# Kernel optimization log

Measured on AMD Instinct MI355X. Metric: run time of the kernel, lower is better.

The kernel has to match this reference:

```python
import jax, jax.numpy as jnp
import numpy as np

H = 8          # attention heads
L = 2          # gnn_layers
D = 256        # embedding_size (= per-head out channels)
NEG_SLOPE = 0.2
LN_EPS = 1e-5


def setup_inputs() -> dict:
    key = jax.random.key(0)
    ks = jax.random.split(key, 10)
    B, N, E = 8, 4096, 131072
    node_embeddings = jax.random.normal(ks[0], (B, N, D), dtype=jnp.float32)
    edges = jax.random.randint(ks[1], (B, 2, E), 0, N, dtype=jnp.int64)
    s = 1.0 / np.sqrt(D)
    W       = jax.random.normal(ks[2], (L, H * D, D), dtype=jnp.float32) * s   # GATConv lin weight
    att_src = jax.random.normal(ks[3], (L, H, D), dtype=jnp.float32) * s
    att_dst = jax.random.normal(ks[4], (L, H, D), dtype=jnp.float32) * s
    gat_bias = jnp.zeros((L, H * D), dtype=jnp.float32)
    lin_W   = jax.random.normal(ks[5], (L, D, H * D), dtype=jnp.float32) * (1.0 / np.sqrt(H * D))
    lin_b   = jnp.zeros((L, D), dtype=jnp.float32)
    ln_gamma = jnp.ones((D,), dtype=jnp.float32)
    ln_beta  = jnp.zeros((D,), dtype=jnp.float32)
    return {"node_embeddings": node_embeddings, "edges": edges, "W": W,
            "att_src": att_src, "att_dst": att_dst, "gat_bias": gat_bias,
            "lin_W": lin_W, "lin_b": lin_b, "ln_gamma": ln_gamma, "ln_beta": ln_beta}


def _gat_conv(x, edge_index, Wl, a_src, a_dst, bias):
    # x: [N, D]; edge_index: [2, E] (row0 = src j, row1 = dst i)
    N = x.shape[0]
    loops = jnp.arange(N, dtype=edge_index.dtype)
    src = jnp.concatenate([edge_index[0], loops])   # PyG add_self_loops=True
    dst = jnp.concatenate([edge_index[1], loops])
    h = (x @ Wl.T).reshape(N, H, D)                 # [N, H, D]
    a_s = jnp.sum(h * a_src, axis=-1)               # [N, H]
    a_d = jnp.sum(h * a_dst, axis=-1)               # [N, H]
    e = jax.nn.leaky_relu(a_s[src] + a_d[dst], NEG_SLOPE)   # [E+N, H]
    # softmax over incoming edges of each destination node
    emax = jax.ops.segment_max(e, dst, num_segments=N)
    ex = jnp.exp(e - emax[dst])
    denom = jax.ops.segment_sum(ex, dst, num_segments=N)
    alpha = ex / (denom[dst] + 1e-16)               # [E+N, H]
    msg = h[src] * alpha[:, :, None]                # [E+N, H, D]
    out = jax.ops.segment_sum(msg, dst, num_segments=N)     # [N, H, D]
    return out.reshape(N, H * D) + bias


def _layer_norm(x, gamma, beta):
    mu = jnp.mean(x, axis=-1, keepdims=True)
    var = jnp.mean(jnp.square(x - mu), axis=-1, keepdims=True)
    return (x - mu) * jax.lax.rsqrt(var + LN_EPS) * gamma + beta


def reference(node_embeddings, edges, W, att_src, att_dst, gat_bias, lin_W, lin_b, ln_gamma, ln_beta):
    def per_graph(x, ei):
        h = x
        for l in range(L):
            res = h
            g = _gat_conv(h, ei, W[l], att_src[l], att_dst[l], gat_bias[l])
            g = g @ lin_W[l].T + lin_b[l]
            g = _layer_norm(g, ln_gamma, ln_beta)
            h = jax.nn.relu(g + res)   # dropout is identity at inference
        return h
    return jax.vmap(per_graph)(node_embeddings, edges)
```

## Files before the change

### kernel.cpp

```cpp
#include <hip/hip_runtime.h>
#include <hip/hip_bf16.h>

#define BB 8
#define NN 4096
#define EE 131072
#define ENL (EE + NN)
#define DD 256
#define HH 8
#define HD 2048
#define NPB (BB * NN)
#define CHUNK 16384
#define CAP 128

typedef __attribute__((ext_vector_type(8))) short bf16x8;
typedef __attribute__((ext_vector_type(4))) float f32x4;

static __device__ __forceinline__ float bf_lo(unsigned int u) { return __uint_as_float(u << 16); }
static __device__ __forceinline__ float bf_hi(unsigned int u) { return __uint_as_float(u & 0xFFFF0000u); }
static __device__ __forceinline__ unsigned short f2bf(float f) {
    __hip_bfloat16 h = __float2bfloat16(f);
    return *reinterpret_cast<unsigned short*>(&h);
}
static __device__ __forceinline__ unsigned int pack2(float a, float b) {
    return ((unsigned)f2bf(b) << 16) | f2bf(a);
}
static __device__ __forceinline__ void load_lds16(const void* g, void* l) {
    __builtin_amdgcn_global_load_lds(
        (const __attribute__((address_space(1))) unsigned int*)(g),
        (__attribute__((address_space(3))) unsigned int*)(l), 16, 0, 0);
}
static __device__ __forceinline__ float rl_f(float v, int lane) {
    return __uint_as_float(__builtin_amdgcn_readlane(__float_as_uint(v), lane));
}

__global__ void k_scatter(const int* __restrict__ edges, int* __restrict__ cnt, int* __restrict__ col) {
    int b = blockIdx.y;
    int idx = blockIdx.x * 256 + threadIdx.x;
    if (idx >= ENL) return;
    int src, dst;
    if (idx < EE) { src = edges[b*2*EE + idx]; dst = edges[b*2*EE + EE + idx]; }
    else { src = dst = idx - EE; }
    int g = b * NN + dst;
    int pos = atomicAdd(&cnt[g], 1);
    if (pos < CAP) col[(size_t)g * CAP + pos] = src;
}

__global__ __launch_bounds__(256) void k_prepA(const float* __restrict__ W, const float* __restrict__ linW,
                                               unsigned short* __restrict__ M2t,
                                               const float* __restrict__ asrc, const float* __restrict__ adst,
                                               float* __restrict__ wsatt, float* __restrict__ wdatt) {
    __shared__ float red[2][4][64];
    int bx = blockIdx.x;
    if (bx < 512) {
        int cb = bx & 31, h = (bx >> 5) & 7, l = bx >> 8;
        int d = threadIdx.x;
        const float* Bp = W + ((size_t)l * HD + h * DD) * DD;
        const float* Ap = linW + ((size_t)l * DD + cb * 8) * HD + h * DD;
        float acc[8] = {};
        for (int o = 0; o < DD; ++o) {
            float w = Bp[(size_t)o * DD + d];
            #pragma unroll
            for (int c = 0; c < 8; ++c)
                acc[c] = fmaf(Ap[(size_t)c * HD + o], w, acc[c]);
        }
        #pragma unroll
        for (int c = 0; c < 8; ++c)
            M2t[((size_t)l * DD + cb * 8 + c) * HD + h * DD + d] = f2bf(acc[c]);
    } else {
        int idx = bx - 512;
        int kb = idx & 3, h = (idx >> 2) & 7, l = idx >> 5;
        int k = threadIdx.x & 63, dg = threadIdx.x >> 6;
        float accs = 0.f, accd = 0.f;
        #pragma unroll 4
        for (int dd = 0; dd < 64; ++dd) {
            int d = dg * 64 + dd;
            float w = W[((size_t)l * HD + h * DD + d) * DD + kb * 64 + k];
            accs = fmaf(asrc[(l*HH + h)*DD + d], w, accs);
            accd = fmaf(adst[(l*HH + h)*DD + d], w, accd);
        }
        red[0][dg][k] = accs; red[1][dg][k] = accd;
        __syncthreads();
        int t = threadIdx.x;
        if (t < 64)
            wsatt[(l*HH + h)*DD + kb*64 + t] = red[0][0][t] + red[0][1][t] + red[0][2][t] + red[0][3][t];
        else if (t < 128) {
            int kk = t - 64;
            wdatt[(l*HH + h)*DD + kb*64 + kk] = red[1][0][kk] + red[1][1][kk] + red[1][2][kk] + red[1][3][kk];
        }
    }
}

__global__ __launch_bounds__(256) void k_prepB(const float* __restrict__ gbias, const float* __restrict__ linW,
                                               const float* __restrict__ linb, float* __restrict__ bias2,
                                               const float* __restrict__ ws, const float* __restrict__ wd,
                                               unsigned short* __restrict__ frag) {
    int bx = blockIdx.x;
    if (bx < 128) {
        int wv = threadIdx.x >> 6, lane = threadIdx.x & 63;
        int o = bx * 4 + wv;
        int l = o >> 8, c = o & 255;
        const float4* g4 = (const float4*)(gbias + l * HD);
        const float4* w4 = (const float4*)(linW + (size_t)l * DD * HD + (size_t)c * HD);
        float acc = 0.f;
        #pragma unroll
        for (int j = 0; j < 8; ++j) {
            float4 g = g4[j * 64 + lane]; float4 w = w4[j * 64 + lane];
            acc += g.x * w.x + g.y * w.y + g.z * w.z + g.w * w.w;
        }
        #pragma unroll
        for (int msk = 1; msk < 64; msk <<= 1) acc += __shfl_xor(acc, msk);
        if (lane == 0) bias2[o] = acc + linb[o];
    } else {
        int idx = bx - 128;
        int l = idx >> 1;
        int t = (idx & 1) * 256 + threadIdx.x;
        int ks = t >> 6, lane = t & 63, c = lane & 15, q = lane >> 4;
        #pragma unroll
        for (int j = 0; j < 8; ++j) {
            int k = ks * 32 + q * 8 + j;
            float v = (c < 8) ? ws[(l*HH + c)*DD + k] : wd[(l*HH + (c-8))*DD + k];
            frag[((size_t)l * 512 + t) * 8 + j] = f2bf(v);
        }
    }
}

__global__ void k_tobf(const float* __restrict__ X, uint2* __restrict__ xb2) {
    int idx = blockIdx.x * 256 + threadIdx.x;
    float4 v = *(const float4*)(X + (size_t)idx * 4);
    uint2 o; o.x = pack2(v.x, v.y); o.y = pack2(v.z, v.w);
    xb2[idx] = o;
}

__global__ __launch_bounds__(256) void k_attn_mfma(const unsigned short* __restrict__ xb,
                                                   const unsigned short* __restrict__ attfrag,
                                                   float* __restrict__ a_s, float* __restrict__ a_d) {
    int tid = threadIdx.x;
    int wv = tid >> 6, lane = tid & 63;
    int m0 = blockIdx.x * 64 + wv * 16;
    int c = lane & 15, q = lane >> 4;
    const unsigned short* arow = xb + (size_t)(m0 + c) * DD;
    f32x4 acc = (f32x4){0.f, 0.f, 0.f, 0.f};
    #pragma unroll
    for (int ks = 0; ks < 8; ++ks) {
        bf16x8 af = *(const bf16x8*)(arow + ks * 32 + q * 8);
        bf16x8 bf = *(const bf16x8*)(attfrag + (size_t)(ks * 64 + lane) * 8);
        acc = __builtin_amdgcn_mfma_f32_16x16x32_bf16(af, bf, acc, 0, 0, 0);
    }
    #pragma unroll
    for (int rg = 0; rg < 4; ++rg) {
        int row = m0 + q * 4 + rg;
        if (c < 8) a_s[row * 8 + c] = acc[rg];
        else       a_d[row * 8 + (c - 8)] = acc[rg];
    }
}

__global__ __launch_bounds__(256) void k_agg_y(const int* __restrict__ cnt, const int* __restrict__ col,
                                               const float* __restrict__ a_s, const float* __restrict__ a_d,
                                               const uint2* __restrict__ xb2, uint2* __restrict__ y2,
                                               int node0) {
    int wave = threadIdx.x >> 6, lane = threadIdx.x & 63;
    int blk = blockIdx.x;
    int xcd = blk & 7, q = blk >> 3;
    int gl = xcd >> 1;
    int sub = ((xcd & 1) << 9) | q;
    int g = node0 + gl * NN + sub * 4 + wave;
    int b = g >> 12;
    int re = cnt[g];
    const int* cl = col + (size_t)g * CAP;
    int gb = b * NN;
    int hl = lane & 7, slot = lane >> 3;
    float adh = a_d[(size_t)g * 8 + hl];
    float acc[8][4] = {};
    float sacc = 0.f;
    for (int e0 = 0; e0 < re; e0 += 8) {
        int e = e0 + slot;
        bool valid = e < re;
        int srcl = valid ? cl[e] : 0;
        float w = 0.f;
        if (valid) {
            float xs = a_s[(size_t)(gb + srcl) * 8 + hl] + adh;
            xs = (xs > 0.f) ? xs : 0.2f * xs;
            w = __expf(xs);
        }
        sacc += w;
        if (e0 + 8 <= re) {
            #pragma unroll
            for (int i = 0; i < 8; ++i) {
                int s = __builtin_amdgcn_readlane(srcl, i * 8);
                uint2 u = xb2[(size_t)(gb + s) * 64 + lane];
                float x0 = bf_lo(u.x), x1 = bf_hi(u.x), x2 = bf_lo(u.y), x3 = bf_hi(u.y);
                #pragma unroll
                for (int h = 0; h < 8; ++h) {
                    float wh = rl_f(w, i * 8 + h);
                    acc[h][0] = fmaf(wh, x0, acc[h][0]);
                    acc[h][1] = fmaf(wh, x1, acc[h][1]);
                    acc[h][2] = fmaf(wh, x2, acc[h][2]);
                    acc[h][3] = fmaf(wh, x3, acc[h][3]);
                }
            }
        } else {
            int cntl = re - e0;
            for (int i = 0; i < cntl; ++i) {
                int s = __builtin_amdgcn_readlane(srcl, i * 8);
                uint2 u = xb2[(size_t)(gb + s) * 64 + lane];
                float x0 = bf_lo(u.x), x1 = bf_hi(u.x), x2 = bf_lo(u.y), x3 = bf_hi(u.y);
                #pragma unroll
                for (int h = 0; h < 8; ++h) {
                    float wh = rl_f(w, i * 8 + h);
                    acc[h][0] = fmaf(wh, x0, acc[h][0]);
                    acc[h][1] = fmaf(wh, x1, acc[h][1]);
                    acc[h][2] = fmaf(wh, x2, acc[h][2]);
                    acc[h][3] = fmaf(wh, x3, acc[h][3]);
                }
            }
        }
    }
    sacc += __shfl_xor(sacc, 8);
    sacc += __shfl_xor(sacc, 16);
    sacc += __shfl_xor(sacc, 32);
    float rinv = 1.f / (sacc + 1e-16f);
    uint2* yr = y2 + (size_t)(g - node0) * 512 + lane;
    #pragma unroll
    for (int h = 0; h < 8; ++h) {
        float rh = rl_f(rinv, h);
        uint2 o;
        o.x = pack2(acc[h][0] * rh, acc[h][1] * rh);
        o.y = pack2(acc[h][2] * rh, acc[h][3] * rh);
        yr[h * 64] = o;
    }
}

__global__ __launch_bounds__(512) void k_gemm_ln(const unsigned short* __restrict__ Yb,
                                                 const unsigned short* __restrict__ Bt,
                                                 const float* __restrict__ bias2,
                                                 const float* __restrict__ gamma,
                                                 const float* __restrict__ beta,
                                                 const float* __restrict__ res,
                                                 float* __restrict__ out,
                                                 unsigned int* __restrict__ xb,
                                                 int node0) {
    __shared__ char lds[81920];
    int tid = threadIdx.x;
    int wv = tid >> 6, lane = tid & 63;
    int m0 = blockIdx.x * 64;
    int c = lane & 15, q = lane >> 4;
    f32x4 acc[4][2];
    #pragma unroll
    for (int mf = 0; mf < 4; ++mf)
        #pragma unroll
        for (int nf = 0; nf < 2; ++nf) acc[mf][nf] = (f32x4){0.f, 0.f, 0.f, 0.f};

    for (int kt = 0; kt < HD; kt += 128) {
        #pragma unroll
        for (int it = 0; it < 2; ++it) {
            int ci = it * 512 + wv * 64 + lane;
            int row = ci >> 4, j = ci & 15, jp = j ^ (row & 15);
            load_lds16(Yb + (size_t)(m0 + row) * HD + kt + jp * 8, lds + it * 8192 + wv * 1024);
        }
        #pragma unroll
        for (int it = 0; it < 8; ++it) {
            int ci = it * 512 + wv * 64 + lane;
            int row = ci >> 4, j = ci & 15, jp = j ^ (row & 15);
            load_lds16(Bt + (size_t)row * HD + kt + jp * 8, lds + 16384 + it * 8192 + wv * 1024);
        }
        __syncthreads();
        #pragma unroll
        for (int ks = 0; ks < 4; ++ks) {
            int kb = ks * 64 + (q << 4);
            bf16x8 af[4], bfr[2];
            #pragma unroll
            for (int mf = 0; mf < 4; ++mf) {
                int r = mf * 16 + c;
                af[mf] = *(const bf16x8*)(lds + r * 256 + (kb ^ ((r & 15) << 4)));
            }
            #pragma unroll
            for (int nf = 0; nf < 2; ++nf) {
                int nr = wv * 32 + nf * 16 + c;
                bfr[nf] = *(const bf16x8*)(lds + 16384 + nr * 256 + (kb ^ ((nr & 15) << 4)));
            }
            #pragma unroll
            for (int mf = 0; mf < 4; ++mf)
                #pragma unroll
                for (int nf = 0; nf < 2; ++nf)
                    acc[mf][nf] = __builtin_amdgcn_mfma_f32_16x16x32_bf16(af[mf], bfr[nf], acc[mf][nf], 0, 0, 0);
        }
        __syncthreads();
    }

    float2* lnbuf = (float2*)lds;
    float2* musd  = (float2*)(lds + 4096);
    float b2[2], gmv[2], btv[2];
    #pragma unroll
    for (int nf = 0; nf < 2; ++nf) {
        int colx = wv * 32 + nf * 16 + c;
        b2[nf] = bias2[colx]; gmv[nf] = gamma[colx]; btv[nf] = beta[colx];
    }
    #pragma unroll
    for (int mf = 0; mf < 4; ++mf)
        #pragma unroll
        for (int nf = 0; nf < 2; ++nf)
            #pragma unroll
            for (int rg = 0; rg < 4; ++rg)
                acc[mf][nf][rg] += b2[nf];
    #pragma unroll
    for (int mf = 0; mf < 4; ++mf) {
        #pragma unroll
        for (int rg = 0; rg < 4; ++rg) {
            float s = 0.f, ss = 0.f;
            #pragma unroll
            for (int nf = 0; nf < 2; ++nf) { float v = acc[mf][nf][rg]; s += v; ss += v * v; }
            #pragma unroll
            for (int msk = 1; msk < 16; msk <<= 1) { s += __shfl_xor(s, msk); ss += __shfl_xor(ss, msk); }
            if (c == 0) lnbuf[(mf * 16 + q * 4 + rg) * 8 + wv] = make_float2(s, ss);
        }
    }
    __syncthreads();
    if (tid < 64) {
        float s = 0.f, ss = 0.f;
        #pragma unroll
        for (int w = 0; w < 8; ++w) { float2 p = lnbuf[tid * 8 + w]; s += p.x; ss += p.y; }
        float mu = s * (1.f / 256.f);
        float var = ss * (1.f / 256.f) - mu * mu;
        musd[tid] = make_float2(mu, rsqrtf(var + 1e-5f));
    }
    __syncthreads();
    #pragma unroll
    for (int mf = 0; mf < 4; ++mf) {
        #pragma unroll
        for (int rg = 0; rg < 4; ++rg) {
            int row = mf * 16 + q * 4 + rg;
            float2 ms = musd[row];
            size_t grow = (size_t)(node0 + m0 + row);
            #pragma unroll
            for (int nf = 0; nf < 2; ++nf) {
                int colx = wv * 32 + nf * 16 + c;
                float o = (acc[mf][nf][rg] - ms.x) * ms.y * gmv[nf] + btv[nf] + res[grow * DD + colx];
                o = fmaxf(o, 0.f);
                out[grow * DD + colx] = o;
                float nb = __shfl_xor(o, 1);
                if (!(c & 1)) xb[grow * 128 + (colx >> 1)] = pack2(o, nb);
            }
        }
    }
}

extern "C" void kernel_launch(void* const* d_in, const int* in_sizes, int n_in,
                              void* d_out, int out_size, void* d_ws, size_t ws_size,
                              hipStream_t stream) {
    const float* emb   = (const float*)d_in[0];
    const int*   edges = (const int*)d_in[1];
    const float* W     = (const float*)d_in[2];
    const float* asrc  = (const float*)d_in[3];
    const float* adst  = (const float*)d_in[4];
    const float* gbias = (const float*)d_in[5];
    const float* linW  = (const float*)d_in[6];
    const float* linb  = (const float*)d_in[7];
    const float* gam   = (const float*)d_in[8];
    const float* bet   = (const float*)d_in[9];
    float* out = (float*)d_out;

    char* ws = (char*)d_ws;
    uint2*          y2      = (uint2*)(ws + 0);
    uint2*          xb2     = (uint2*)(ws + 67108864);
    unsigned short* M2t     = (unsigned short*)(ws + 83886080);
    float*          wsatt   = (float*)(ws + 85983232);
    float*          wdatt   = (float*)(ws + 85999616);
    float*          bias2   = (float*)(ws + 86016000);
    float*          a_s     = (float*)(ws + 86018048);
    float*          a_d     = (float*)(ws + 87066624);
    int*            cnt     = (int*)(ws + 88115200);
    int*            colx    = (int*)(ws + 88246272);
    unsigned short* attfrag = (unsigned short*)(ws + 105023488);

    hipMemsetAsync(cnt, 0, NPB * sizeof(int), stream);
    k_scatter<<<dim3((ENL + 255) / 256, BB), 256, 0, stream>>>(edges, cnt, colx);
    k_prepA<<<dim3(576), 256, 0, stream>>>(W, linW, M2t, asrc, adst, wsatt, wdatt);
    k_prepB<<<dim3(132), 256, 0, stream>>>(gbias, linW, linb, bias2, wsatt, wdatt, attfrag);
    k_tobf<<<dim3(NPB * 64 / 256), 256, 0, stream>>>(emb, xb2);

    for (int l = 0; l < 2; ++l) {
        const float* X = (l == 0) ? emb : out;
        k_attn_mfma<<<dim3(NPB / 64), 256, 0, stream>>>((const unsigned short*)xb2,
                                                        attfrag + (size_t)l * 4096, a_s, a_d);
        for (int cc = 0; cc < 2; ++cc) {
            int node0 = cc * CHUNK;
            k_agg_y<<<dim3(CHUNK / 4), 256, 0, stream>>>(cnt, colx, a_s, a_d, xb2, y2, node0);
            k_gemm_ln<<<dim3(CHUNK / 64), 512, 0, stream>>>((const unsigned short*)y2,
                                                            M2t + (size_t)l * DD * HD, bias2 + l * DD,
                                                            gam, bet, X, out,
                                                            (unsigned int*)xb2, node0);
        }
    }
}
```

Before: 573.2 us.

## Double-buffer GEMM K-tiles and batch gather loads in aggregation

The GEMM+LayerNorm kernel now uses two LDS buffers with 64-wide K tiles, so loading the next tile overlaps with the MFMA work on the current one and there is one barrier per tile instead of two. The LayerNorm scratch moves to a separate region so it does not overlap the buffers. The aggregation kernel splits off full groups of 8 edges and issues all 8 gathered row loads before the exp and FMA work, to raise memory-level parallelism. The costs are more LDS per block (possibly lower occupancy), more registers for the prefetched rows, and smaller K steps.

```diff
diff --git a/kernel.cpp b/kernel.cpp
--- a/kernel.cpp
+++ b/kernel.cpp
@@ -172,8 +172,36 @@
     float adh = a_d[(size_t)g * 8 + hl];
     float acc[8][4] = {};
     float sacc = 0.f;
-    for (int e0 = 0; e0 < re; e0 += 8) {
-        int e = e0 + slot;
+    int nfull = re & ~7;
+    for (int e0 = 0; e0 < nfull; e0 += 8) {
+        int srcl = cl[e0 + slot];
+        float sg = a_s[(size_t)(gb + srcl) * 8 + hl];
+        int ss[8];
+        #pragma unroll
+        for (int i = 0; i < 8; ++i) ss[i] = __builtin_amdgcn_readlane(srcl, i * 8);
+        uint2 u[8];
+        #pragma unroll
+        for (int i = 0; i < 8; ++i)
+            u[i] = xb2[(size_t)(gb + ss[i]) * 64 + lane];
+        float xs = sg + adh;
+        xs = (xs > 0.f) ? xs : 0.2f * xs;
+        float w = __expf(xs);
+        sacc += w;
+        #pragma unroll
+        for (int i = 0; i < 8; ++i) {
+            float x0 = bf_lo(u[i].x), x1 = bf_hi(u[i].x), x2 = bf_lo(u[i].y), x3 = bf_hi(u[i].y);
+            #pragma unroll
+            for (int h = 0; h < 8; ++h) {
+                float wh = rl_f(w, i * 8 + h);
+                acc[h][0] = fmaf(wh, x0, acc[h][0]);
+                acc[h][1] = fmaf(wh, x1, acc[h][1]);
+                acc[h][2] = fmaf(wh, x2, acc[h][2]);
+                acc[h][3] = fmaf(wh, x3, acc[h][3]);
+            }
+        }
+    }
+    if (nfull < re) {
+        int e = nfull + slot;
         bool valid = e < re;
         int srcl = valid ? cl[e] : 0;
         float w = 0.f;
@@ -183,35 +211,18 @@
             w = __expf(xs);
         }
         sacc += w;
-        if (e0 + 8 <= re) {
-            #pragma unroll
-            for (int i = 0; i < 8; ++i) {
-                int s = __builtin_amdgcn_readlane(srcl, i * 8);
-                uint2 u = xb2[(size_t)(gb + s) * 64 + lane];
-                float x0 = bf_lo(u.x), x1 = bf_hi(u.x), x2 = bf_lo(u.y), x3 = bf_hi(u.y);
-                #pragma unroll
-                for (int h = 0; h < 8; ++h) {
-                    float wh = rl_f(w, i * 8 + h);
-                    acc[h][0] = fmaf(wh, x0, acc[h][0]);
-                    acc[h][1] = fmaf(wh, x1, acc[h][1]);
-                    acc[h][2] = fmaf(wh, x2, acc[h][2]);
-                    acc[h][3] = fmaf(wh, x3, acc[h][3]);
-                }
-            }
-        } else {
-            int cntl = re - e0;
-            for (int i = 0; i < cntl; ++i) {
-                int s = __builtin_amdgcn_readlane(srcl, i * 8);
-                uint2 u = xb2[(size_t)(gb + s) * 64 + lane];
-                float x0 = bf_lo(u.x), x1 = bf_hi(u.x), x2 = bf_lo(u.y), x3 = bf_hi(u.y);
-                #pragma unroll
-                for (int h = 0; h < 8; ++h) {
-                    float wh = rl_f(w, i * 8 + h);
-                    acc[h][0] = fmaf(wh, x0, acc[h][0]);
-                    acc[h][1] = fmaf(wh, x1, acc[h][1]);
-                    acc[h][2] = fmaf(wh, x2, acc[h][2]);
-                    acc[h][3] = fmaf(wh, x3, acc[h][3]);
-                }
+        int cntl = re - nfull;
+        for (int i = 0; i < cntl; ++i) {
+            int s = __builtin_amdgcn_readlane(srcl, i * 8);
+            uint2 u = xb2[(size_t)(gb + s) * 64 + lane];
+            float x0 = bf_lo(u.x), x1 = bf_hi(u.x), x2 = bf_lo(u.y), x3 = bf_hi(u.y);
+            #pragma unroll
+            for (int h = 0; h < 8; ++h) {
+                float wh = rl_f(w, i * 8 + h);
+                acc[h][0] = fmaf(wh, x0, acc[h][0]);
+                acc[h][1] = fmaf(wh, x1, acc[h][1]);
+                acc[h][2] = fmaf(wh, x2, acc[h][2]);
+                acc[h][3] = fmaf(wh, x3, acc[h][3]);
             }
         }
     }
@@ -239,7 +250,7 @@
                                                  float* __restrict__ out,
                                                  unsigned int* __restrict__ xb,
                                                  int node0) {
-    __shared__ char lds[81920];
+    __shared__ char lds[86528];
     int tid = threadIdx.x;
     int wv = tid >> 6, lane = tid & 63;
     int m0 = blockIdx.x * 64;
@@ -250,45 +261,60 @@
         #pragma unroll
         for (int nf = 0; nf < 2; ++nf) acc[mf][nf] = (f32x4){0.f, 0.f, 0.f, 0.f};
 
-    for (int kt = 0; kt < HD; kt += 128) {
-        #pragma unroll
-        for (int it = 0; it < 2; ++it) {
-            int ci = it * 512 + wv * 64 + lane;
-            int row = ci >> 4, j = ci & 15, jp = j ^ (row & 15);
-            load_lds16(Yb + (size_t)(m0 + row) * HD + kt + jp * 8, lds + it * 8192 + wv * 1024);
-        }
-        #pragma unroll
-        for (int it = 0; it < 8; ++it) {
-            int ci = it * 512 + wv * 64 + lane;
-            int row = ci >> 4, j = ci & 15, jp = j ^ (row & 15);
-            load_lds16(Bt + (size_t)row * HD + kt + jp * 8, lds + 16384 + it * 8192 + wv * 1024);
-        }
+    #define STAGE(BUF, KT) do {                                                        \
+        int row_ = tid >> 3, j_ = tid & 7, jp_ = j_ ^ (row_ & 7);                      \
+        load_lds16(Yb + (size_t)(m0 + row_) * HD + (KT) + jp_ * 8,                     \
+                   lds + (BUF) * 40960 + wv * 1024);                                   \
+        _Pragma("unroll")                                                              \
+        for (int it_ = 0; it_ < 4; ++it_) {                                            \
+            int ci_ = it_ * 512 + tid;                                                 \
+            int br_ = ci_ >> 3, bj_ = ci_ & 7, bjp_ = bj_ ^ (br_ & 7);                 \
+            load_lds16(Bt + (size_t)br_ * HD + (KT) + bjp_ * 8,                        \
+                       lds + (BUF) * 40960 + 8192 + it_ * 8192 + wv * 1024);           \
+        }                                                                              \
+    } while (0)
+
+    #define COMPUTE(BUF) do {                                                          \
+        const char* Ab_ = lds + (BUF) * 40960;                                         \
+        const char* Bb_ = lds + (BUF) * 40960 + 8192;                                  \
+        _Pragma("unroll")                                                              \
+        for (int ks = 0; ks < 2; ++ks) {                                               \
+            int kb = ks * 64 + (q << 4);                                               \
+            bf16x8 af[4], bfr[2];                                                      \
+            _Pragma("unroll")                                                          \
+            for (int mf = 0; mf < 4; ++mf) {                                           \
+                int r = mf * 16 + c;                                                   \
+                af[mf] = *(const bf16x8*)(Ab_ + r * 128 + (kb ^ ((r & 7) << 4)));      \
+            }                                                                          \
+            _Pragma("unroll")                                                          \
+            for (int nf = 0; nf < 2; ++nf) {                                           \
+                int nr = wv * 32 + nf * 16 + c;                                        \
+                bfr[nf] = *(const bf16x8*)(Bb_ + nr * 128 + (kb ^ ((nr & 7) << 4)));   \
+            }                                                                          \
+            _Pragma("unroll")                                                          \
+            for (int mf = 0; mf < 4; ++mf)                                             \
+                _Pragma("unroll")                                                      \
+                for (int nf = 0; nf < 2; ++nf)                                         \
+                    acc[mf][nf] = __builtin_amdgcn_mfma_f32_16x16x32_bf16(             \
+                        af[mf], bfr[nf], acc[mf][nf], 0, 0, 0);                        \
+        }                                                                              \
+    } while (0)
+
+    STAGE(0, 0);
+    __syncthreads();
+    for (int t = 0; t < 32; t += 2) {
+        if (t + 1 < 32) STAGE(1, (t + 1) * 64);
+        COMPUTE(0);
         __syncthreads();
-        #pragma unroll
-        for (int ks = 0; ks < 4; ++ks) {
-            int kb = ks * 64 + (q << 4);
-            bf16x8 af[4], bfr[2];
-            #pragma unroll
-            for (int mf = 0; mf < 4; ++mf) {
-                int r = mf * 16 + c;
-                af[mf] = *(const bf16x8*)(lds + r * 256 + (kb ^ ((r & 15) << 4)));
-            }
-            #pragma unroll
-            for (int nf = 0; nf < 2; ++nf) {
-                int nr = wv * 32 + nf * 16 + c;
-                bfr[nf] = *(const bf16x8*)(lds + 16384 + nr * 256 + (kb ^ ((nr & 15) << 4)));
-            }
-            #pragma unroll
-            for (int mf = 0; mf < 4; ++mf)
-                #pragma unroll
-                for (int nf = 0; nf < 2; ++nf)
-                    acc[mf][nf] = __builtin_amdgcn_mfma_f32_16x16x32_bf16(af[mf], bfr[nf], acc[mf][nf], 0, 0, 0);
-        }
+        if (t + 2 < 32) STAGE(0, (t + 2) * 64);
+        COMPUTE(1);
         __syncthreads();
     }
-
-    float2* lnbuf = (float2*)lds;
-    float2* musd  = (float2*)(lds + 4096);
+    #undef STAGE
+    #undef COMPUTE
+
+    float2* lnbuf = (float2*)(lds + 81920);
+    float2* musd  = (float2*)(lds + 86016);
     float b2[2], gmv[2], btv[2];
     #pragma unroll
     for (int nf = 0; nf < 2; ++nf) {
```

Result: faster. 543.8 us (-5.1%).
